# Kernel optimization log

Hardware: AMD Instinct MI355X
Metric: run time of the kernel (lower is better)

Reference implementation:

```python
import jax, jax.numpy as jnp
import numpy as np

N = 4096
NUM_FEATURES = 1870
HIDDEN = 256
EMBED = 16
ALPHA = 0.2
NEG_BIG = -9e15
EPS = 1e-12


def setup_inputs() -> dict:
    key = jax.random.key(0)
    ks = jax.random.split(key, 9)
    x = jax.random.normal(ks[0], (N, NUM_FEATURES), dtype=jnp.float32)
    # sparse-ish binary adjacency mask (avg degree ~ 41) with self loops
    adj = (jax.random.uniform(ks[1], (N, N)) < 0.01).astype(jnp.float32)
    adj = jnp.maximum(adj, jnp.eye(N, dtype=jnp.float32))
    M = jax.random.uniform(ks[2], (N, N), dtype=jnp.float32)
    s1 = 1.0 / np.sqrt(NUM_FEATURES)
    s2 = 1.0 / np.sqrt(HIDDEN)
    W1 = jax.random.normal(ks[3], (NUM_FEATURES, HIDDEN), dtype=jnp.float32) * s1
    a_self1 = jax.random.normal(ks[4], (HIDDEN, 1), dtype=jnp.float32) * s2
    a_neighs1 = jax.random.normal(ks[5], (HIDDEN, 1), dtype=jnp.float32) * s2
    W2 = jax.random.normal(ks[6], (HIDDEN, EMBED), dtype=jnp.float32) * s2
    a_self2 = jax.random.normal(ks[7], (EMBED, 1), dtype=jnp.float32) / np.sqrt(EMBED)
    a_neighs2 = jax.random.normal(ks[8], (EMBED, 1), dtype=jnp.float32) / np.sqrt(EMBED)
    return {"x": x, "adj": adj, "M": M, "W1": W1, "a_self1": a_self1,
            "a_neighs1": a_neighs1, "W2": W2, "a_self2": a_self2, "a_neighs2": a_neighs2}


def gat_layer(x, adj, M, W, a_self, a_neighs, alpha):
    h = x @ W                                  # [N, out]
    f_self = h @ a_self                        # [N, 1]
    f_neigh = h @ a_neighs                     # [N, 1]
    e = jax.nn.leaky_relu((f_self + f_neigh.T) * M, negative_slope=alpha)  # [N, N]
    e = jnp.where(adj > 0, e, NEG_BIG)
    att = jax.nn.softmax(e, axis=1)            # row-stochastic over neighbors
    return jax.nn.elu(att @ h)                 # [N, out]


def reference(x, adj, M, W1, a_self1, a_neighs1, W2, a_self2, a_neighs2):
    h = gat_layer(x, adj, M, W1, a_self1, a_neighs1, ALPHA)
    h = gat_layer(h, adj, M, W2, a_self2, a_neighs2, ALPHA)
    # F.normalize(h, p=2, dim=1): divide by max(norm, eps)
    norm = jnp.maximum(jnp.linalg.norm(h, axis=1, keepdims=True), EPS)
    z = h / norm                               # [N, EMBED]
    A_pred = jax.nn.sigmoid(z @ z.T)           # [N, N]
    return (A_pred, z)
```

## Files before the change

### kernel.cpp

```cpp
#include <hip/hip_runtime.h>
#include <math.h>

#define NN 4096
#define NFEAT 1870
#define KB2 2048
#define KSPLIT 8
#define KCHUNK 256
#define BK 32
#define HID 256
#define EMB 16
#define MAXDEG 128

typedef __attribute__((ext_vector_type(8))) _Float16 f16x8;
typedef __attribute__((ext_vector_type(4))) float f32x4;

__device__ __forceinline__ ushort f2h(float f) {
    _Float16 h = (_Float16)f;
    return __builtin_bit_cast(ushort, h);
}

__device__ __forceinline__ void gload_lds16(const void* g, void* l) {
    __builtin_amdgcn_global_load_lds(
        (const __attribute__((address_space(1))) unsigned int*)g,
        (__attribute__((address_space(3))) unsigned int*)l, 16, 0, 0);
}

__global__ __launch_bounds__(256) void prep_kernel(
    const float* __restrict__ adj, unsigned long long* __restrict__ masks,
    const float* __restrict__ W1, ushort* __restrict__ Wh)
{
    const int b = blockIdx.x;
    const int tid = threadIdx.x;
    if (b < NN / 4) {
        const int wv = tid >> 6, lane = tid & 63;
        const int row = b * 4 + wv;
        const float* arow = adj + (size_t)row * NN;
        unsigned long long* mrow = masks + (size_t)row * 64;
#pragma unroll
        for (int i = 0; i < 16; ++i) {
            float4 v = *(const float4*)&arow[(size_t)(i * 64 + lane) * 4];
            unsigned long long b0 = __ballot(v.x > 0.f);
            unsigned long long b1 = __ballot(v.y > 0.f);
            unsigned long long b2 = __ballot(v.z > 0.f);
            unsigned long long b3 = __ballot(v.w > 0.f);
            if (lane == 0) {
                mrow[i * 4 + 0] = b0; mrow[i * 4 + 1] = b1;
                mrow[i * 4 + 2] = b2; mrow[i * 4 + 3] = b3;
            }
        }
    } else {
        __shared__ float t[64][65];
        const int bb = b - NN / 4;
        const int k0 = (bb & 31) * 64, n0 = (bb >> 5) * 64;
        const int kk = tid >> 2, c4 = (tid & 3) * 16;
#pragma unroll
        for (int j = 0; j < 4; ++j) {
            int k = k0 + kk;
            float4 v = make_float4(0.f, 0.f, 0.f, 0.f);
            if (k < NFEAT) v = *(const float4*)&W1[(size_t)k * HID + n0 + c4 + j * 4];
            t[kk][c4 + j * 4 + 0] = v.x; t[kk][c4 + j * 4 + 1] = v.y;
            t[kk][c4 + j * 4 + 2] = v.z; t[kk][c4 + j * 4 + 3] = v.w;
        }
        __syncthreads();
        const int on = tid >> 2, ok4 = (tid & 3) * 16;
#pragma unroll
        for (int j = 0; j < 4; ++j) {
            ushort hh[4];
#pragma unroll
            for (int i = 0; i < 4; ++i)
                hh[i] = f2h(t[ok4 + j * 4 + i][on]);
            size_t o = (size_t)(n0 + on) * KB2 + k0 + ok4 + j * 4;
            *(ushort4*)&Wh[o] = *(ushort4*)hh;
        }
    }
}

__global__ __launch_bounds__(256, 2) void gemm_xw1(
    const float* __restrict__ Xg,
    const ushort* __restrict__ Bg,
    float* __restrict__ Cpart)
{
    __shared__ ushort Ah[128 * BK];
    __shared__ ushort Bh[128 * BK];
    const int tid = threadIdx.x;
    const int lane = tid & 63;
    const int w = tid >> 6;
    const int wr = w >> 1, wc = w & 1;
    const int row0 = blockIdx.x * 128;
    const int col0 = blockIdx.y * 128;
    const int kbeg = blockIdx.z * KCHUNK;
    const int fr = lane & 15, fs = lane >> 4;

    const int ar = tid >> 1;
    const int ah = tid & 1;
    const size_t abase = (size_t)(row0 + ar) * NFEAT;
    const size_t XMAX = (size_t)NN * NFEAT - 8;

    f32x4 acc[4][4] = {};

    for (int ks = 0; ks < KCHUNK / BK; ++ks) {
        const int k0 = kbeg + ks * BK;
        __syncthreads();
#pragma unroll
        for (int i = 0; i < 2; ++i) {
            int idx = i * 256 + tid;
            int r = idx >> 2, t = idx & 3;
            int kslot = (t ^ (r & 3)) * 8;
            gload_lds16(&Bg[(size_t)(col0 + r) * KB2 + k0 + kslot], &Bh[idx * 8]);
        }
#pragma unroll
        for (int s = 0; s < 2; ++s) {
            int sk = ah * 2 + s;
            size_t gi = abase + k0 + sk * 8;
            if (gi > XMAX) gi = XMAX;
            float2 v0 = *(const float2*)&Xg[gi];
            float2 v1 = *(const float2*)&Xg[gi + 2];
            float2 v2 = *(const float2*)&Xg[gi + 4];
            float2 v3 = *(const float2*)&Xg[gi + 6];
            ushort u[8];
            u[0] = f2h(v0.x); u[1] = f2h(v0.y);
            u[2] = f2h(v1.x); u[3] = f2h(v1.y);
            u[4] = f2h(v2.x); u[5] = f2h(v2.y);
            u[6] = f2h(v3.x); u[7] = f2h(v3.y);
            *(int4*)&Ah[ar * 32 + ((sk ^ (ar & 3)) * 8)] = *(int4*)u;
        }
        __syncthreads();
        f16x8 af[4], bf[4];
#pragma unroll
        for (int m = 0; m < 4; ++m) {
            int r = wr * 64 + m * 16 + fr;
            af[m] = *(const f16x8*)&Ah[r * BK + ((fs ^ (r & 3)) * 8)];
        }
#pragma unroll
        for (int n = 0; n < 4; ++n) {
            int r = wc * 64 + n * 16 + fr;
            bf[n] = *(const f16x8*)&Bh[r * BK + ((fs ^ (r & 3)) * 8)];
        }
#pragma unroll
        for (int m = 0; m < 4; ++m)
#pragma unroll
            for (int n = 0; n < 4; ++n)
                acc[m][n] = __builtin_amdgcn_mfma_f32_16x16x32_f16(
                    af[m], bf[n], acc[m][n], 0, 0, 0);
    }
    float* Cp = Cpart + (size_t)blockIdx.z * NN * HID;
#pragma unroll
    for (int m = 0; m < 4; ++m)
#pragma unroll
        for (int n = 0; n < 4; ++n)
#pragma unroll
            for (int r = 0; r < 4; ++r) {
                int row = row0 + wr * 64 + m * 16 + fs * 4 + r;
                int col = col0 + wc * 64 + n * 16 + fr;
                Cp[(size_t)row * HID + col] = acc[m][n][r];
            }
}

__global__ __launch_bounds__(256) void reduce_h1f_kernel(
    const float* __restrict__ part, float* __restrict__ h1,
    const float* __restrict__ a_s, const float* __restrict__ a_n,
    float* __restrict__ fs, float* __restrict__ fn)
{
    const int tid = threadIdx.x, wv = tid >> 6, lane = tid & 63;
    const int row = blockIdx.x * 4 + wv;
    const int d0 = lane * 4;
    const size_t o = (size_t)row * HID + d0;
    float4 s = *(const float4*)&part[o];
#pragma unroll
    for (int ch = 1; ch < KSPLIT; ++ch) {
        float4 p = *(const float4*)&part[(size_t)ch * NN * HID + o];
        s.x += p.x; s.y += p.y; s.z += p.z; s.w += p.w;
    }
    *(float4*)&h1[o] = s;
    float4 as4 = *(const float4*)&a_s[d0];
    float4 an4 = *(const float4*)&a_n[d0];
    float ps = s.x * as4.x + s.y * as4.y + s.z * as4.z + s.w * as4.w;
    float pn = s.x * an4.x + s.y * an4.y + s.z * an4.z + s.w * an4.w;
#pragma unroll
    for (int off = 32; off > 0; off >>= 1) {
        ps += __shfl_down(ps, off, 64);
        pn += __shfl_down(pn, off, 64);
    }
    if (lane == 0) { fs[row] = ps; fn[row] = pn; }
}

__global__ __launch_bounds__(256) void spmm1_kernel(
    const unsigned long long* __restrict__ masks,
    const float* __restrict__ Mmat,
    const float* __restrict__ fs, const float* __restrict__ fn,
    const float* __restrict__ h1,
    int* __restrict__ nnz, int* __restrict__ gidx, float* __restrict__ MgG,
    float* __restrict__ g1)
{
    __shared__ float p_s[MAXDEG];
    __shared__ int j_s[MAXDEG];
    __shared__ float wred[4], wsum[4];
    __shared__ int cnt_s;
    const int row = blockIdx.x;
    const int tid = threadIdx.x;
    const int lane = tid & 63, wv = tid >> 6;

    if (wv == 0) {
        unsigned long long m = masks[(size_t)row * 64 + lane];
        const int c = __popcll(m);
        int incl = c;
#pragma unroll
        for (int off = 1; off < 64; off <<= 1) {
            int y = __shfl_up(incl, off, 64);
            if (lane >= off) incl += y;
        }
        int off = incl - c;
        const int i = lane >> 2, cc = lane & 3;
        while (m) {
            int l = __ffsll(m) - 1;
            m &= m - 1;
            if (off < MAXDEG) j_s[off] = (i * 64 + l) * 4 + cc;
            ++off;
        }
        if (lane == 63) {
            int t = min(incl, MAXDEG);
            cnt_s = t;
            nnz[row] = t;
        }
    }
    __syncthreads();
    const int cnt = cnt_s;
    const float fsi = fs[row];

    float lmax = -3.0e38f;
    for (int s = tid; s < cnt; s += 256) {
        int j = j_s[s];
        float mv = Mmat[(size_t)row * NN + j];
        gidx[(size_t)row * MAXDEG + s] = j;
        MgG[(size_t)row * MAXDEG + s] = mv;
        float e = (fsi + fn[j]) * mv;
        e = (e > 0.f) ? e : 0.2f * e;
        p_s[s] = e;
        lmax = fmaxf(lmax, e);
    }
#pragma unroll
    for (int off = 32; off > 0; off >>= 1)
        lmax = fmaxf(lmax, __shfl_down(lmax, off, 64));
    if (lane == 0) wred[wv] = lmax;
    __syncthreads();
    const float m = fmaxf(fmaxf(wred[0], wred[1]), fmaxf(wred[2], wred[3]));

    float lsum = 0.f;
    for (int s = tid; s < cnt; s += 256) {
        float p = __expf(p_s[s] - m);
        p_s[s] = p;
        lsum += p;
    }
#pragma unroll
    for (int off = 32; off > 0; off >>= 1)
        lsum += __shfl_down(lsum, off, 64);
    if (lane == 0) wsum[wv] = lsum;
    __syncthreads();
    const float inv = 1.f / (wsum[0] + wsum[1] + wsum[2] + wsum[3]);

    float acc = 0.f;
#pragma unroll 4
    for (int s = 0; s < cnt; ++s)
        acc += p_s[s] * h1[(size_t)j_s[s] * HID + tid];
    float v = acc * inv;
    v = (v > 0.f) ? v : (__expf(v) - 1.f);
    g1[(size_t)row * HID + tid] = v;
}

__global__ __launch_bounds__(256) void gemm_h2_kernel(
    const float* __restrict__ g1, const float* __restrict__ W2,
    const float* __restrict__ a_s2, const float* __restrict__ a_n2,
    float* __restrict__ h2, float* __restrict__ fs2, float* __restrict__ fn2)
{
    __shared__ float Ws[256][16];
    __shared__ float Gs[16][257];
    const int tid = threadIdx.x;
    const int row0 = blockIdx.x * 16;
#pragma unroll
    for (int i = 0; i < 16; ++i) {
        int idx = tid + i * 256;
        Ws[idx >> 4][idx & 15] = W2[idx];
    }
#pragma unroll
    for (int i = 0; i < 16; ++i) {
        int idx = tid + i * 256;
        Gs[idx >> 8][idx & 255] = g1[(size_t)(row0 + (idx >> 8)) * HID + (idx & 255)];
    }
    __syncthreads();
    const int r = tid >> 4, c = tid & 15;
    float acc = 0.f;
#pragma unroll 8
    for (int k = 0; k < 256; ++k)
        acc += Gs[r][k] * Ws[k][c];
    h2[(size_t)(row0 + r) * EMB + c] = acc;

    float ps = acc * a_s2[c];
    float pn = acc * a_n2[c];
#pragma unroll
    for (int off = 1; off < 16; off <<= 1) {
        ps += __shfl_xor(ps, off, 64);
        pn += __shfl_xor(pn, off, 64);
    }
    if (c == 0) { fs2[row0 + r] = ps; fn2[row0 + r] = pn; }
}

__global__ __launch_bounds__(256) void spmm2_kernel(
    const int* __restrict__ nnz, const int* __restrict__ gidx,
    const float* __restrict__ Mg,
    const float* __restrict__ fs, const float* __restrict__ fn,
    const float* __restrict__ h2, float* __restrict__ z)
{
    __shared__ float p_s[4][MAXDEG];
    __shared__ int j_s[4][MAXDEG];
    const int tid = threadIdx.x;
    const int wv = tid >> 6, lane = tid & 63;
    const int row = blockIdx.x * 4 + wv;
    const int cnt = nnz[row];
    const float fsi = fs[row];

    float lmax = -3.0e38f;
    for (int s = lane; s < cnt; s += 64) {
        int j = gidx[(size_t)row * MAXDEG + s];
        j_s[wv][s] = j;
        float e = (fsi + fn[j]) * Mg[(size_t)row * MAXDEG + s];
        e = (e > 0.f) ? e : 0.2f * e;
        p_s[wv][s] = e;
        lmax = fmaxf(lmax, e);
    }
#pragma unroll
    for (int off = 1; off < 64; off <<= 1)
        lmax = fmaxf(lmax, __shfl_xor(lmax, off, 64));

    float lsum = 0.f;
    for (int s = lane; s < cnt; s += 64) {
        float p = __expf(p_s[wv][s] - lmax);
        p_s[wv][s] = p;
        lsum += p;
    }
#pragma unroll
    for (int off = 1; off < 64; off <<= 1)
        lsum += __shfl_xor(lsum, off, 64);
    const float inv = 1.f / lsum;

    const int s0 = lane >> 4, d = lane & 15;
    float acc = 0.f;
    for (int s = s0; s < cnt; s += 4)
        acc += p_s[wv][s] * h2[(size_t)j_s[wv][s] * EMB + d];
    acc += __shfl_xor(acc, 16, 64);
    acc += __shfl_xor(acc, 32, 64);

    float v = acc * inv;
    v = (v > 0.f) ? v : (__expf(v) - 1.f);
    float ss = v * v;
#pragma unroll
    for (int off = 1; off < 16; off <<= 1)
        ss += __shfl_xor(ss, off, 64);
    float zn = v / fmaxf(sqrtf(ss), 1e-12f);
    if (lane < 16) z[(size_t)row * EMB + lane] = zn;
}

__global__ __launch_bounds__(256) void apred_kernel(
    const float* __restrict__ z, float* __restrict__ out)
{
    __shared__ float zr[64][20];
    __shared__ float zc[64][20];
    const int tid = threadIdx.x;
    const int r0 = blockIdx.y * 64, c0 = blockIdx.x * 64;
#pragma unroll
    for (int i = 0; i < 4; ++i) {
        int idx = tid + i * 256;
        int rr = idx >> 4, d = idx & 15;
        zr[rr][d] = z[(size_t)(r0 + rr) * EMB + d];
        zc[rr][d] = z[(size_t)(c0 + rr) * EMB + d];
    }
    __syncthreads();
    const int tx = tid & 15, ty = tid >> 4;
    float rb[4][16], cb[4][16];
#pragma unroll
    for (int i = 0; i < 4; ++i)
#pragma unroll
        for (int d = 0; d < 16; ++d) {
            rb[i][d] = zr[ty * 4 + i][d];
            cb[i][d] = zc[tx * 4 + i][d];
        }
#pragma unroll
    for (int i = 0; i < 4; ++i) {
        float4 o;
        float v[4];
#pragma unroll
        for (int j = 0; j < 4; ++j) {
            float s = 0.f;
#pragma unroll
            for (int d = 0; d < 16; ++d) s += rb[i][d] * cb[j][d];
            v[j] = 1.f / (1.f + __expf(-s));
        }
        o.x = v[0]; o.y = v[1]; o.z = v[2]; o.w = v[3];
        *reinterpret_cast<float4*>(
            &out[(size_t)(r0 + ty * 4 + i) * NN + c0 + tx * 4]) = o;
    }
}

extern "C" void kernel_launch(void* const* d_in, const int* in_sizes, int n_in,
                              void* d_out, int out_size, void* d_ws, size_t ws_size,
                              hipStream_t stream)
{
    const float* x    = (const float*)d_in[0];
    const float* adj  = (const float*)d_in[1];
    const float* Mm   = (const float*)d_in[2];
    const float* W1   = (const float*)d_in[3];
    const float* a_s1 = (const float*)d_in[4];
    const float* a_n1 = (const float*)d_in[5];
    const float* W2   = (const float*)d_in[6];
    const float* a_s2 = (const float*)d_in[7];
    const float* a_n2 = (const float*)d_in[8];

    float* out = (float*)d_out;
    float* z   = out + (size_t)NN * NN;
    float* part = out;

    char* w = (char*)d_ws;
    float* h1    = (float*)w;  w += (size_t)NN * HID * 4;
    float* g1    = (float*)w;  w += (size_t)NN * HID * 4;
    ushort* W1Th = (ushort*)w; w += (size_t)HID * KB2 * 2;
    float* h2    = (float*)w;  w += (size_t)NN * EMB * 4;
    unsigned long long* masks = (unsigned long long*)w;
    w += (size_t)NN * 64 * 8;
    int*   nnzp  = (int*)w;    w += NN * 4;
    int*   gidx  = (int*)w;    w += (size_t)NN * MAXDEG * 4;
    float* Mg    = (float*)w;  w += (size_t)NN * MAXDEG * 4;
    float* fs1   = (float*)w;  w += NN * 4;
    float* fn1   = (float*)w;  w += NN * 4;
    float* fs2   = (float*)w;  w += NN * 4;
    float* fn2   = (float*)w;  w += NN * 4;

    prep_kernel<<<NN / 4 + 128, 256, 0, stream>>>(adj, masks, W1, W1Th);

    gemm_xw1<<<dim3(32, 2, KSPLIT), 256, 0, stream>>>(x, W1Th, part);
    reduce_h1f_kernel<<<NN / 4, 256, 0, stream>>>(part, h1, a_s1, a_n1, fs1, fn1);
    spmm1_kernel<<<NN, 256, 0, stream>>>(masks, Mm, fs1, fn1, h1,
                                         nnzp, gidx, Mg, g1);

    gemm_h2_kernel<<<256, 256, 0, stream>>>(g1, W2, a_s2, a_n2, h2, fs2, fn2);
    spmm2_kernel<<<NN / 4, 256, 0, stream>>>(nnzp, gidx, Mg, fs2, fn2, h2, z);

    apred_kernel<<<dim3(64, 64), 256, 0, stream>>>(z, out);
}
```

Measured before the change: 96.68 us.

## Fuse adjacency mask build into split-K GEMM launch and halve K-split

Mask building from the adjacency matrix moves out of the prep kernel and into the X·W1 GEMM launch as extra blocks. The bandwidth-bound read of the dense adj matrix can then overlap with the MFMA-bound GEMM instead of running before it. The W1 transpose/half conversion stays as its own small kernel. The split-K factor drops from 8 to 4 with longer K chunks, which halves the partial-sum buffers written and later reduced. The cost is fewer GEMM blocks for parallelism and heavier per-block work, which could leave CUs underused.

```diff
diff --git a/kernel.cpp b/kernel.cpp
--- a/kernel.cpp
+++ b/kernel.cpp
@@ -4,9 +4,10 @@
 #define NN 4096
 #define NFEAT 1870
 #define KB2 2048
-#define KSPLIT 8
-#define KCHUNK 256
+#define KSPLIT 4
+#define KCHUNK 512
 #define BK 32
+#define GEMMB 256
 #define HID 256
 #define EMB 16
 #define MAXDEG 128
@@ -25,15 +26,50 @@
         (__attribute__((address_space(3))) unsigned int*)l, 16, 0, 0);
 }
 
-__global__ __launch_bounds__(256) void prep_kernel(
-    const float* __restrict__ adj, unsigned long long* __restrict__ masks,
+__global__ __launch_bounds__(256) void w1t_kernel(
     const float* __restrict__ W1, ushort* __restrict__ Wh)
 {
-    const int b = blockIdx.x;
-    const int tid = threadIdx.x;
-    if (b < NN / 4) {
+    __shared__ float t[64][65];
+    const int bb = blockIdx.x;
+    const int tid = threadIdx.x;
+    const int k0 = (bb & 31) * 64, n0 = (bb >> 5) * 64;
+    const int kk = tid >> 2, c4 = (tid & 3) * 16;
+#pragma unroll
+    for (int j = 0; j < 4; ++j) {
+        int k = k0 + kk;
+        float4 v = make_float4(0.f, 0.f, 0.f, 0.f);
+        if (k < NFEAT) v = *(const float4*)&W1[(size_t)k * HID + n0 + c4 + j * 4];
+        t[kk][c4 + j * 4 + 0] = v.x; t[kk][c4 + j * 4 + 1] = v.y;
+        t[kk][c4 + j * 4 + 2] = v.z; t[kk][c4 + j * 4 + 3] = v.w;
+    }
+    __syncthreads();
+    const int on = tid >> 2, ok4 = (tid & 3) * 16;
+#pragma unroll
+    for (int j = 0; j < 4; ++j) {
+        ushort hh[4];
+#pragma unroll
+        for (int i = 0; i < 4; ++i)
+            hh[i] = f2h(t[ok4 + j * 4 + i][on]);
+        size_t o = (size_t)(n0 + on) * KB2 + k0 + ok4 + j * 4;
+        *(ushort4*)&Wh[o] = *(ushort4*)hh;
+    }
+}
+
+__global__ __launch_bounds__(256, 2) void gemm_ext_kernel(
+    const float* __restrict__ Xg,
+    const ushort* __restrict__ Bg,
+    float* __restrict__ Cpart,
+    const float* __restrict__ adj,
+    unsigned long long* __restrict__ masks)
+{
+    __shared__ ushort Ah[128 * BK];
+    __shared__ ushort Bh[128 * BK];
+    const int tid = threadIdx.x;
+
+    if (blockIdx.x >= GEMMB) {
+        const int bb = blockIdx.x - GEMMB;
         const int wv = tid >> 6, lane = tid & 63;
-        const int row = b * 4 + wv;
+        const int row = bb * 4 + wv;
         const float* arow = adj + (size_t)row * NN;
         unsigned long long* mrow = masks + (size_t)row * 64;
 #pragma unroll
@@ -48,47 +84,19 @@
                 mrow[i * 4 + 2] = b2; mrow[i * 4 + 3] = b3;
             }
         }
-    } else {
-        __shared__ float t[64][65];
-        const int bb = b - NN / 4;
-        const int k0 = (bb & 31) * 64, n0 = (bb >> 5) * 64;
-        const int kk = tid >> 2, c4 = (tid & 3) * 16;
-#pragma unroll
-        for (int j = 0; j < 4; ++j) {
-            int k = k0 + kk;
-            float4 v = make_float4(0.f, 0.f, 0.f, 0.f);
-            if (k < NFEAT) v = *(const float4*)&W1[(size_t)k * HID + n0 + c4 + j * 4];
-            t[kk][c4 + j * 4 + 0] = v.x; t[kk][c4 + j * 4 + 1] = v.y;
-            t[kk][c4 + j * 4 + 2] = v.z; t[kk][c4 + j * 4 + 3] = v.w;
-        }
-        __syncthreads();
-        const int on = tid >> 2, ok4 = (tid & 3) * 16;
-#pragma unroll
-        for (int j = 0; j < 4; ++j) {
-            ushort hh[4];
-#pragma unroll
-            for (int i = 0; i < 4; ++i)
-                hh[i] = f2h(t[ok4 + j * 4 + i][on]);
-            size_t o = (size_t)(n0 + on) * KB2 + k0 + ok4 + j * 4;
-            *(ushort4*)&Wh[o] = *(ushort4*)hh;
-        }
-    }
-}
-
-__global__ __launch_bounds__(256, 2) void gemm_xw1(
-    const float* __restrict__ Xg,
-    const ushort* __restrict__ Bg,
-    float* __restrict__ Cpart)
-{
-    __shared__ ushort Ah[128 * BK];
-    __shared__ ushort Bh[128 * BK];
-    const int tid = threadIdx.x;
+        return;
+    }
+
+    const int bid = blockIdx.x;
     const int lane = tid & 63;
     const int w = tid >> 6;
     const int wr = w >> 1, wc = w & 1;
-    const int row0 = blockIdx.x * 128;
-    const int col0 = blockIdx.y * 128;
-    const int kbeg = blockIdx.z * KCHUNK;
+    const int mgrp = bid >> 3;
+    const int cgrp = (bid >> 2) & 1;
+    const int z    = bid & 3;
+    const int row0 = mgrp * 128;
+    const int col0 = cgrp * 128;
+    const int kbeg = z * KCHUNK;
     const int fr = lane & 15, fs = lane >> 4;
 
     const int ar = tid >> 1;
@@ -143,7 +151,7 @@
                 acc[m][n] = __builtin_amdgcn_mfma_f32_16x16x32_f16(
                     af[m], bf[n], acc[m][n], 0, 0, 0);
     }
-    float* Cp = Cpart + (size_t)blockIdx.z * NN * HID;
+    float* Cp = Cpart + (size_t)z * NN * HID;
 #pragma unroll
     for (int m = 0; m < 4; ++m)
 #pragma unroll
@@ -433,9 +441,11 @@
     float* fs2   = (float*)w;  w += NN * 4;
     float* fn2   = (float*)w;  w += NN * 4;
 
-    prep_kernel<<<NN / 4 + 128, 256, 0, stream>>>(adj, masks, W1, W1Th);
-
-    gemm_xw1<<<dim3(32, 2, KSPLIT), 256, 0, stream>>>(x, W1Th, part);
+    w1t_kernel<<<128, 256, 0, stream>>>(W1, W1Th);
+
+    gemm_ext_kernel<<<GEMMB + NN / 4, 256, 0, stream>>>(
+        x, W1Th, part, adj, masks);
+
     reduce_h1f_kernel<<<NN / 4, 256, 0, stream>>>(part, h1, a_s1, a_n1, fs1, fn1);
     spmm1_kernel<<<NN, 256, 0, stream>>>(masks, Mm, fs1, fn1, h1,
                                          nnzp, gidx, Mg, g1);
```

New measurement: 99.90 us. +3.3%, slower.
